# Performance work log

Measured on AMD Instinct MI355X. Metric: run time of the kernel, lower is better.

## Reference

```python
import jax, jax.numpy as jnp
import numpy as np

# ViT-Base-ish encoder: 256x256 img, patch 8 -> N=1024 tokens, dim 768, 8 layers
B, C, H, W = 8, 3, 256, 256
P, D, DEPTH, HEADS, DH, MLP = 8, 768, 8, 12, 64, 3072
N = (H // P) * (W // P)
INNER = HEADS * DH  # 768
EPS = 1e-5


def setup_inputs() -> dict:
    key = jax.random.key(0)
    ks = jax.random.split(key, 8)
    s = lambda i, shape, scale=0.02: jax.random.normal(ks[i], shape, jnp.float32) * scale
    return {
        "x": s(0, (B, C, H, W), 1.0),
        "w_conv": s(1, (D, C, P, P)),          # OIHW conv kernel (patch embed)
        "b_conv": jnp.zeros((D,), jnp.float32),
        "pos_emb": s(2, (1, N, D)),
        "ln1_w": jnp.ones((DEPTH, D), jnp.float32),
        "ln1_b": jnp.zeros((DEPTH, D), jnp.float32),
        "qkv_w": s(3, (DEPTH, D, 3 * INNER)),  # stored [in,out]; Linear has no bias
        "out_w": s(4, (DEPTH, INNER, D)),
        "out_b": jnp.zeros((DEPTH, D), jnp.float32),
        "ln2_w": jnp.ones((DEPTH, D), jnp.float32),
        "ln2_b": jnp.zeros((DEPTH, D), jnp.float32),
        "w1": s(5, (DEPTH, D, MLP)),
        "b1": jnp.zeros((DEPTH, MLP), jnp.float32),
        "w2": s(6, (DEPTH, MLP, D)),
        "b2": jnp.zeros((DEPTH, D), jnp.float32),
    }


def _layernorm(x, w, b):
    m = jnp.mean(x, axis=-1, keepdims=True)
    v = jnp.mean(jnp.square(x - m), axis=-1, keepdims=True)
    return (x - m) * jax.lax.rsqrt(v + EPS) * w + b


def _encoder(x, w_conv, b_conv, pos_emb, ln1_w, ln1_b, qkv_w, out_w, out_b,
             ln2_w, ln2_b, w1, b1, w2, b2):
    # PatchEmbed: strided conv -> flatten(2).transpose(1,2)
    h = jax.lax.conv_general_dilated(
        x, w_conv, window_strides=(P, P), padding='VALID',
        dimension_numbers=('NCHW', 'OIHW', 'NCHW'))
    h = h + b_conv[None, :, None, None]
    h = h.reshape(B, D, N).transpose(0, 2, 1)  # [B, N, D]
    h = h + pos_emb
    scale = DH ** -0.5

    def block(h, p):
        l1w, l1b, qkvw, ow, ob, l2w, l2b, W1, B1, W2, B2 = p
        # PreNorm + MHSA
        y = _layernorm(h, l1w, l1b)
        qkv = y @ qkvw                                   # [B,N,3*INNER]
        q, k, v = jnp.split(qkv, 3, axis=-1)
        split_heads = lambda t: t.reshape(B, N, HEADS, DH).transpose(0, 2, 1, 3)
        q, k, v = split_heads(q), split_heads(k), split_heads(v)
        attn = jax.nn.softmax(jnp.einsum('bhnd,bhmd->bhnm', q, k) * scale, axis=-1)
        o = jnp.einsum('bhnm,bhmd->bhnd', attn, v)
        o = o.transpose(0, 2, 1, 3).reshape(B, N, INNER)
        h = h + (o @ ow + ob)
        # PreNorm + FFN (exact GELU, dropout=0)
        y = _layernorm(h, l2w, l2b)
        h = h + (jax.nn.gelu(y @ W1 + B1, approximate=False) @ W2 + B2)
        return h, None

    h, _ = jax.lax.scan(block, h, (ln1_w, ln1_b, qkv_w, out_w, out_b,
                                   ln2_w, ln2_b, w1, b1, w2, b2))
    return h


def reference(x, w_conv, b_conv, pos_emb, ln1_w, ln1_b, qkv_w, out_w, out_b,
              ln2_w, ln2_b, w1, b1, w2, b2):
    return _encoder(x, w_conv, b_conv, pos_emb, ln1_w, ln1_b, qkv_w, out_w,
                    out_b, ln2_w, ln2_b, w1, b1, w2, b2)
```

## Files before the change

kernel.cpp:

```cpp
#include <hip/hip_runtime.h>
#include <math.h>

#define BATCH 8
#define CIN 3
#define HIMG 256
#define WIMG 256
#define PATCH 8
#define DMODEL 768
#define DEPTH 8
#define HEADS 12
#define DHEAD 64
#define MLPDIM 3072
#define NTOK 1024
#define INNER 768
#define MROWS (BATCH * NTOK)
#define QKVS (3 * INNER)
#define KPATCH (CIN * PATCH * PATCH)
#define LNEPS 1e-5f
#define PSTR 72
#define QSCALE 0.18033688011112042f

typedef __attribute__((ext_vector_type(8))) short short8;
typedef __attribute__((ext_vector_type(4))) float v4f;

__device__ __forceinline__ float b2f(unsigned short u) {
  union { unsigned int i; float f; } x;
  x.i = (unsigned int)u << 16;
  return x.f;
}
__device__ __forceinline__ unsigned short f2b(float f) {
  union { float f; unsigned int i; } x;
  x.f = f;
  unsigned int r = x.i + 0x7FFFu + ((x.i >> 16) & 1u);
  return (unsigned short)(r >> 16);
}
__device__ __forceinline__ unsigned int pkrh(float a, float b) {
  union { float f; unsigned int u; } x, y;
  x.f = a; y.f = b;
  return ((x.u + 0x8000u) >> 16) | ((y.u + 0x8000u) & 0xFFFF0000u);
}

#define GLL(gp, lp)                                                     \
  __builtin_amdgcn_global_load_lds(                                     \
      (const __attribute__((address_space(1))) void*)(gp),              \
      (__attribute__((address_space(3))) void*)(lp), 16, 0, 0)

__global__ __launch_bounds__(256) void cast_kernel(
    const float* __restrict__ src, unsigned short* __restrict__ dst, int n) {
  int i = blockIdx.x * 256 + threadIdx.x;
  if (i < n) dst[i] = f2b(src[i]);
}

__global__ __launch_bounds__(256) void transpose_cast_kernel(
    const float* __restrict__ src, unsigned short* __restrict__ dst, int R,
    int C) {
  __shared__ unsigned short t[32][33];
  src += (size_t)blockIdx.z * R * C;
  dst += (size_t)blockIdx.z * R * C;
  int c0 = blockIdx.x * 32, r0 = blockIdx.y * 32;
  int tx = threadIdx.x & 31, ty = threadIdx.x >> 5;
#pragma unroll
  for (int u = 0; u < 4; ++u) {
    int r = r0 + ty + u * 8;
    t[ty + u * 8][tx] = f2b(src[(size_t)r * C + c0 + tx]);
  }
  __syncthreads();
#pragma unroll
  for (int u = 0; u < 4; ++u) {
    int c = c0 + ty + u * 8;
    dst[(size_t)c * R + r0 + tx] = t[tx][ty + u * 8];
  }
}

__global__ __launch_bounds__(256) void vtrans_kernel(
    const unsigned short* __restrict__ qkv, unsigned short* __restrict__ vt) {
  __shared__ unsigned short t[32][33];
  int k0 = blockIdx.x * 32;
  int d0 = blockIdx.y * 32;
  int bh = blockIdx.z;
  int b = bh / HEADS, h = bh % HEADS;
  int tx = threadIdx.x & 31, ty = threadIdx.x >> 5;
  const unsigned short* src =
      qkv + (size_t)(b * NTOK) * QKVS + 2 * INNER + h * DHEAD;
#pragma unroll
  for (int u = 0; u < 4; ++u)
    t[ty + u * 8][tx] = src[(size_t)(k0 + ty + u * 8) * QKVS + d0 + tx];
  __syncthreads();
  unsigned short* dst = vt + ((size_t)bh * DHEAD + d0) * NTOK + k0;
#pragma unroll
  for (int u = 0; u < 4; ++u)
    dst[(size_t)(ty + u * 8) * NTOK + tx] = t[tx][ty + u * 8];
}

__global__ __launch_bounds__(256) void im2col_kernel(
    const float* __restrict__ x, unsigned short* __restrict__ A) {
  int idx = blockIdx.x * 256 + threadIdx.x;
  if (idx >= MROWS * KPATCH) return;
  int m = idx / KPATCH, k = idx % KPATCH;
  int b = m / NTOK, n = m % NTOK;
  int ph = n / 32, pw = n % 32;
  int c = k / 64, r = k % 64;
  int py = r / 8, px = r % 8;
  A[idx] =
      f2b(x[((size_t)(b * CIN + c) * HIMG + ph * 8 + py) * WIMG + pw * 8 + px]);
}

template <int EPI, int OB, int MT>
__global__ __launch_bounds__(256) void mfma_gemm_kernel(
    const unsigned short* __restrict__ Ag, const unsigned short* __restrict__ Bt,
    const float* __restrict__ bias, const float* __restrict__ res,
    void* __restrict__ Cg, int Mdim, int Ndim, int Kdim) {
  constexpr int MI = MT / 32;
  constexpr int RA = MT / 4;
  constexpr int NGA = RA / 16;
  __shared__ __align__(16) unsigned short Asm[MT * 32];
  __shared__ __align__(16) unsigned short Bsm[128 * 32];
  int tid = threadIdx.x;
  int lane = tid & 63, wv = tid >> 6;

  int Nt = Ndim / 128;
  int mchunk = (Mdim / MT) >> 3;
  int bid = blockIdx.x;
  int xcd = bid & 7;
  int j = bid >> 3;
  int m0 = (xcd * mchunk + j / Nt) * MT;
  int n0 = (j % Nt) * 128;

  v4f acc[MI][4] = {};
  int srow = lane >> 2, schunk = (lane & 3) * 8;

  const unsigned short* Aw = Ag + (size_t)(m0 + RA * wv + srow) * Kdim + schunk;
  const unsigned short* Bw = Bt + (size_t)(n0 + 32 * wv + srow) * Kdim + schunk;
  unsigned short* As0 = Asm + (RA * wv) * 32;
  unsigned short* Bs0 = Bsm + (32 * wv) * 32;

  int quad = lane >> 4, lr = lane & 15;
  int fr0 = (wv >> 1) * (MI * 16);
  int fc0 = (wv & 1) * 64;
  const unsigned short* Afr = Asm + (fr0 + lr) * 32 + quad * 8;
  const unsigned short* Bfr = Bsm + (fc0 + lr) * 32 + quad * 8;

  for (int k0 = 0; k0 < Kdim; k0 += 32) {
    GLL(Aw + k0, As0);
    if (NGA == 2) GLL(Aw + k0 + (size_t)16 * Kdim, As0 + 16 * 32);
    GLL(Bw + k0, Bs0);
    GLL(Bw + k0 + (size_t)16 * Kdim, Bs0 + 16 * 32);
    __syncthreads();
    short8 af[MI], bf[4];
#pragma unroll
    for (int i = 0; i < MI; ++i) af[i] = *(const short8*)(Afr + i * 16 * 32);
#pragma unroll
    for (int n = 0; n < 4; ++n) bf[n] = *(const short8*)(Bfr + n * 16 * 32);
#pragma unroll
    for (int i = 0; i < MI; ++i)
#pragma unroll
      for (int n = 0; n < 4; ++n)
        acc[i][n] = __builtin_amdgcn_mfma_f32_16x16x32_bf16(af[i], bf[n],
                                                            acc[i][n], 0, 0, 0);
    __syncthreads();
  }

  float* Cf = (float*)Cg;
  unsigned short* Cb = (unsigned short*)Cg;
#pragma unroll
  for (int i = 0; i < MI; ++i) {
#pragma unroll
    for (int n = 0; n < 4; ++n) {
      int ncol = n0 + fc0 + 16 * n + lr;
#pragma unroll
      for (int reg = 0; reg < 4; ++reg) {
        int mrow = m0 + fr0 + 16 * i + quad * 4 + reg;
        float v = acc[i][n][reg];
        if (EPI == 2 || EPI == 3 || EPI == 4) v += bias[ncol];
        if (EPI == 2) v += res[(size_t)mrow * Ndim + ncol];
        if (EPI == 3) {
          float u = v * (0.7978845608028654f + 0.035677408136300125f * v * v);
          float a = fminf(fmaxf(u * 2.8853900817779268f, -60.f), 60.f);
          float E = __builtin_amdgcn_exp2f(a);
          v = v * E * __builtin_amdgcn_rcpf(E + 1.0f);
        }
        if (EPI == 4) v += res[(size_t)(mrow % NTOK) * Ndim + ncol];
        if (EPI == 5 && ncol < INNER) v *= QSCALE;
        if (OB)
          Cb[(size_t)mrow * Ndim + ncol] = f2b(v);
        else
          Cf[(size_t)mrow * Ndim + ncol] = v;
      }
    }
  }
}

__global__ __launch_bounds__(256) void ln_kernel(
    const float* __restrict__ x, const float* __restrict__ w,
    const float* __restrict__ b, unsigned short* __restrict__ y) {
  int row = blockIdx.x;
  const float* xr = x + (size_t)row * DMODEL;
  unsigned short* yr = y + (size_t)row * DMODEL;
  int tid = threadIdx.x;
  float v0 = xr[tid], v1 = xr[tid + 256], v2 = xr[tid + 512];
  float s = v0 + v1 + v2;
  __shared__ float red[4];
#pragma unroll
  for (int off = 32; off >= 1; off >>= 1) s += __shfl_xor(s, off, 64);
  if ((tid & 63) == 0) red[tid >> 6] = s;
  __syncthreads();
  float mean = (red[0] + red[1] + red[2] + red[3]) * (1.0f / DMODEL);
  float d0 = v0 - mean, d1 = v1 - mean, d2 = v2 - mean;
  float sq = d0 * d0 + d1 * d1 + d2 * d2;
  __syncthreads();
#pragma unroll
  for (int off = 32; off >= 1; off >>= 1) sq += __shfl_xor(sq, off, 64);
  if ((tid & 63) == 0) red[tid >> 6] = sq;
  __syncthreads();
  float var = (red[0] + red[1] + red[2] + red[3]) * (1.0f / DMODEL);
  float rs = rsqrtf(var + LNEPS);
  yr[tid] = f2b(d0 * rs * w[tid] + b[tid]);
  yr[tid + 256] = f2b(d1 * rs * w[tid + 256] + b[tid + 256]);
  yr[tid + 512] = f2b(d2 * rs * w[tid + 512] + b[tid + 512]);
}

__global__ __launch_bounds__(256) void attn_kernel(
    const unsigned short* __restrict__ qkv,
    const unsigned short* __restrict__ vtg, unsigned short* __restrict__ o) {
  __shared__ __align__(16) unsigned short Ks[64 * PSTR];
  __shared__ __align__(16) unsigned short Vs[64 * PSTR];
  __shared__ __align__(16) unsigned short Pl[4][32 * PSTR];
  int tid = threadIdx.x;
  int lane = tid & 63, wv = tid >> 6;
  int quad = lane >> 4, lr = lane & 15;
  int q0 = blockIdx.x * 128, hh = blockIdx.y, bb = blockIdx.z;

  const unsigned short* qg =
      qkv + (size_t)(bb * NTOK + q0 + wv * 32) * QKVS + hh * DHEAD;
  const unsigned short* kg =
      qkv + (size_t)(bb * NTOK) * QKVS + INNER + hh * DHEAD;
  const unsigned short* vg = vtg + (size_t)(bb * HEADS + hh) * DHEAD * NTOK;
  unsigned short* Pw = Pl[wv];

  int srow = lane >> 3, soff = (lane & 7) * 8;

#pragma unroll
  for (int p = 0; p < 4; ++p) {
    int r = p * 8 + srow;
    *(int4*)(Pw + r * PSTR + soff) =
        *(const int4*)(qg + (size_t)r * QKVS + soff);
  }
  short8 qf[2][2];
#pragma unroll
  for (int n = 0; n < 2; ++n)
#pragma unroll
    for (int s = 0; s < 2; ++s)
      qf[n][s] =
          *(const short8*)(Pw + (n * 16 + lr) * PSTR + s * 32 + quad * 8);

  v4f oac[2][4] = {};
  float m_i[2] = {-1e30f, -1e30f};
  float l_i[2] = {0.f, 0.f};

  for (int t = 0; t < NTOK / 64; ++t) {
    __syncthreads();
#pragma unroll
    for (int p = 0; p < 2; ++p) {
      int r = wv * 16 + p * 8 + srow;
      *(int4*)(Ks + r * PSTR + soff) =
          *(const int4*)(kg + (size_t)(t * 64 + r) * QKVS + soff);
      *(int4*)(Vs + r * PSTR + soff) =
          *(const int4*)(vg + (size_t)r * NTOK + t * 64 + soff);
    }
    __syncthreads();

    v4f sac[4][2] = {};
#pragma unroll
    for (int s = 0; s < 2; ++s) {
      short8 kf[4];
#pragma unroll
      for (int mt = 0; mt < 4; ++mt)
        kf[mt] =
            *(const short8*)(Ks + (mt * 16 + lr) * PSTR + s * 32 + quad * 8);
#pragma unroll
      for (int mt = 0; mt < 4; ++mt)
#pragma unroll
        for (int n = 0; n < 2; ++n)
          sac[mt][n] = __builtin_amdgcn_mfma_f32_16x16x32_bf16(
              kf[mt], qf[n][s], sac[mt][n], 0, 0, 0);
    }

#pragma unroll
    for (int n = 0; n < 2; ++n) {
      float mx = -1e30f;
#pragma unroll
      for (int mt = 0; mt < 4; ++mt)
#pragma unroll
        for (int r = 0; r < 4; ++r) mx = fmaxf(mx, sac[mt][n][r]);
      mx = fmaxf(mx, __shfl_xor(mx, 16, 64));
      mx = fmaxf(mx, __shfl_xor(mx, 32, 64));
      float mnew = fmaxf(m_i[n], mx);
      float alpha = __builtin_amdgcn_exp2f(m_i[n] - mnew);
      m_i[n] = mnew;
      float sum = 0.f;
#pragma unroll
      for (int mt = 0; mt < 4; ++mt) {
#pragma unroll
        for (int r = 0; r < 4; ++r) {
          float p = __builtin_amdgcn_exp2f(sac[mt][n][r] - mnew);
          sac[mt][n][r] = p;
          sum += p;
        }
        *(uint2*)(Pw + (n * 16 + lr) * PSTR + mt * 16 + quad * 4) =
            make_uint2(pkrh(sac[mt][n][0], sac[mt][n][1]),
                       pkrh(sac[mt][n][2], sac[mt][n][3]));
      }
      sum += __shfl_xor(sum, 16, 64);
      sum += __shfl_xor(sum, 32, 64);
      l_i[n] = l_i[n] * alpha + sum;
#pragma unroll
      for (int r = 0; r < 4; ++r) {
        float ao = __shfl(alpha, quad * 4 + r, 64);
#pragma unroll
        for (int j = 0; j < 4; ++j) oac[n][j][r] *= ao;
      }
    }

#pragma unroll
    for (int s = 0; s < 2; ++s) {
      short8 pf[2], vf[4];
#pragma unroll
      for (int i = 0; i < 2; ++i)
        pf[i] =
            *(const short8*)(Pw + (i * 16 + lr) * PSTR + s * 32 + quad * 8);
#pragma unroll
      for (int j = 0; j < 4; ++j)
        vf[j] =
            *(const short8*)(Vs + (j * 16 + lr) * PSTR + s * 32 + quad * 8);
#pragma unroll
      for (int i = 0; i < 2; ++i)
#pragma unroll
        for (int j = 0; j < 4; ++j)
          oac[i][j] = __builtin_amdgcn_mfma_f32_16x16x32_bf16(
              pf[i], vf[j], oac[i][j], 0, 0, 0);
    }
  }

  unsigned short* ob =
      o + (size_t)(bb * NTOK + q0 + wv * 32) * INNER + hh * DHEAD;
#pragma unroll
  for (int i = 0; i < 2; ++i) {
    float inv = 1.0f / l_i[i];
#pragma unroll
    for (int r = 0; r < 4; ++r) {
      float il = __shfl(inv, quad * 4 + r, 64);
      int row = i * 16 + quad * 4 + r;
#pragma unroll
      for (int j = 0; j < 4; ++j)
        ob[(size_t)row * INNER + 16 * j + lr] = f2b(oac[i][j][r] * il);
    }
  }
}

extern "C" void kernel_launch(void* const* d_in, const int* in_sizes, int n_in,
                              void* d_out, int out_size, void* d_ws,
                              size_t ws_size, hipStream_t stream) {
  const float* x      = (const float*)d_in[0];
  const float* w_conv = (const float*)d_in[1];
  const float* b_conv = (const float*)d_in[2];
  const float* pos    = (const float*)d_in[3];
  const float* ln1w   = (const float*)d_in[4];
  const float* ln1b   = (const float*)d_in[5];
  const float* qkvw   = (const float*)d_in[6];
  const float* outw   = (const float*)d_in[7];
  const float* outb   = (const float*)d_in[8];
  const float* ln2w   = (const float*)d_in[9];
  const float* ln2b   = (const float*)d_in[10];
  const float* w1     = (const float*)d_in[11];
  const float* b1     = (const float*)d_in[12];
  const float* w2     = (const float*)d_in[13];
  const float* b2     = (const float*)d_in[14];

  char* ws = (char*)d_ws;
  float* outp = (float*)d_out;
  dim3 blk(256);

  float* h            = (float*)(ws + 0);
  unsigned short* big = (unsigned short*)(ws + 25165824);
  unsigned short* y   = (unsigned short*)(ws + 75497472);

  const size_t NEEDED = 214204416;
  bool batched = ws_size >= NEEDED;

  unsigned short *vt, *wc, *wqa, *woa, *w1a, *w2a;
  unsigned short *wq_f, *wo_f, *w1_f, *w2_f;
  if (batched) {
    vt  = (unsigned short*)(ws + 88080384);
    wc  = (unsigned short*)(ws + 100663296);
    wqa = (unsigned short*)(ws + 100958208);
    woa = (unsigned short*)(ws + 129269760);
    w1a = (unsigned short*)(ws + 138706944);
    w2a = (unsigned short*)(ws + 176455680);
    wq_f = wo_f = w1_f = w2_f = nullptr;
  } else {
    wq_f = (unsigned short*)(ws + 88080384);
    wo_f = (unsigned short*)(ws + 91619328);
    w1_f = (unsigned short*)(ws + 92798976);
    w2_f = (unsigned short*)(ws + 97517568);
    wc   = (unsigned short*)(ws + 102236160);
    vt   = (unsigned short*)(ws + 102531072);
    wqa = woa = w1a = w2a = nullptr;
  }

  cast_kernel<<<dim3((DMODEL * KPATCH + 255) / 256), blk, 0, stream>>>(
      w_conv, wc, DMODEL * KPATCH);
  im2col_kernel<<<dim3((MROWS * KPATCH + 255) / 256), blk, 0, stream>>>(x, big);
  mfma_gemm_kernel<4, 0, 64>
      <<<dim3((MROWS / 64) * (DMODEL / 128)), blk, 0, stream>>>(
          big, wc, b_conv, pos, h, MROWS, DMODEL, KPATCH);

  if (batched) {
    transpose_cast_kernel<<<dim3(QKVS / 32, DMODEL / 32, DEPTH), blk, 0,
                            stream>>>(qkvw, wqa, DMODEL, QKVS);
    transpose_cast_kernel<<<dim3(DMODEL / 32, INNER / 32, DEPTH), blk, 0,
                            stream>>>(outw, woa, INNER, DMODEL);
    transpose_cast_kernel<<<dim3(MLPDIM / 32, DMODEL / 32, DEPTH), blk, 0,
                            stream>>>(w1, w1a, DMODEL, MLPDIM);
    transpose_cast_kernel<<<dim3(DMODEL / 32, MLPDIM / 32, DEPTH), blk, 0,
                            stream>>>(w2, w2a, MLPDIM, DMODEL);
  }

  for (int l = 0; l < DEPTH; ++l) {
    unsigned short* wq = batched ? wqa + (size_t)l * DMODEL * QKVS : wq_f;
    unsigned short* wo = batched ? woa + (size_t)l * INNER * DMODEL : wo_f;
    unsigned short* w1t = batched ? w1a + (size_t)l * DMODEL * MLPDIM : w1_f;
    unsigned short* w2t = batched ? w2a + (size_t)l * MLPDIM * DMODEL : w2_f;
    if (!batched) {
      transpose_cast_kernel<<<dim3(QKVS / 32, DMODEL / 32), blk, 0, stream>>>(
          qkvw + (size_t)l * DMODEL * QKVS, wq, DMODEL, QKVS);
    }
    ln_kernel<<<dim3(MROWS), blk, 0, stream>>>(h, ln1w + l * DMODEL,
                                               ln1b + l * DMODEL, y);
    mfma_gemm_kernel<5, 1, 128>
        <<<dim3((MROWS / 128) * (QKVS / 128)), blk, 0, stream>>>(
            y, wq, nullptr, nullptr, big, MROWS, QKVS, DMODEL);
    vtrans_kernel<<<dim3(NTOK / 32, DHEAD / 32, BATCH * HEADS), blk, 0,
                    stream>>>(big, vt);
    attn_kernel<<<dim3(NTOK / 128, HEADS, BATCH), blk, 0, stream>>>(big, vt, y);
    if (!batched) {
      transpose_cast_kernel<<<dim3(DMODEL / 32, INNER / 32), blk, 0, stream>>>(
          outw + (size_t)l * INNER * DMODEL, wo, INNER, DMODEL);
    }
    mfma_gemm_kernel<2, 0, 64>
        <<<dim3((MROWS / 64) * (DMODEL / 128)), blk, 0, stream>>>(
            y, wo, outb + l * DMODEL, h, h, MROWS, DMODEL, INNER);
    ln_kernel<<<dim3(MROWS), blk, 0, stream>>>(h, ln2w + l * DMODEL,
                                               ln2b + l * DMODEL, y);
    if (!batched) {
      transpose_cast_kernel<<<dim3(MLPDIM / 32, DMODEL / 32), blk, 0, stream>>>(
          w1 + (size_t)l * DMODEL * MLPDIM, w1t, DMODEL, MLPDIM);
    }
    mfma_gemm_kernel<3, 1, 128>
        <<<dim3((MROWS / 128) * (MLPDIM / 128)), blk, 0, stream>>>(
            y, w1t, b1 + l * MLPDIM, nullptr, big, MROWS, MLPDIM, DMODEL);
    if (!batched) {
      transpose_cast_kernel<<<dim3(DMODEL / 32, MLPDIM / 32), blk, 0, stream>>>(
          w2 + (size_t)l * MLPDIM * DMODEL, w2t, MLPDIM, DMODEL);
    }
    float* dst = (l == DEPTH - 1) ? outp : h;
    mfma_gemm_kernel<2, 0, 64>
        <<<dim3((MROWS / 64) * (DMODEL / 128)), blk, 0, stream>>>(
            big, w2t, b2 + l * DMODEL, h, dst, MROWS, DMODEL, MLPDIM);
  }
}
```

Measured before the change: 2.543 ms.

## Double GEMM K-tile to 64 with XOR-swizzled LDS layout

The MFMA GEMM now stages a 64-wide K slice per iteration instead of 32, which halves the number of barrier pairs per K loop. The LDS tiles are stored with an XOR swizzle on the 16-byte chunk index, and the fragment reads use the same swizzle, to avoid bank conflicts from the wider row stride. The cost is doubled LDS use per block, which may reduce occupancy, and the kernel now needs Kdim to be a multiple of 64.

Result: faster. 2.215 ms (-12.9%).

```diff
diff --git a/kernel.cpp b/kernel.cpp
--- a/kernel.cpp
+++ b/kernel.cpp
@@ -112,9 +112,9 @@
     void* __restrict__ Cg, int Mdim, int Ndim, int Kdim) {
   constexpr int MI = MT / 32;
   constexpr int RA = MT / 4;
-  constexpr int NGA = RA / 16;
-  __shared__ __align__(16) unsigned short Asm[MT * 32];
-  __shared__ __align__(16) unsigned short Bsm[128 * 32];
+  constexpr int NCA = RA / 8;
+  __shared__ __align__(16) unsigned short Asm[MT * 64];
+  __shared__ __align__(16) unsigned short Bsm[128 * 64];
   int tid = threadIdx.x;
   int lane = tid & 63, wv = tid >> 6;
 
@@ -127,36 +127,46 @@
   int n0 = (j % Nt) * 128;
 
   v4f acc[MI][4] = {};
-  int srow = lane >> 2, schunk = (lane & 3) * 8;
-
-  const unsigned short* Aw = Ag + (size_t)(m0 + RA * wv + srow) * Kdim + schunk;
-  const unsigned short* Bw = Bt + (size_t)(n0 + 32 * wv + srow) * Kdim + schunk;
-  unsigned short* As0 = Asm + (RA * wv) * 32;
-  unsigned short* Bs0 = Bsm + (32 * wv) * 32;
+
+  int sr8 = lane >> 3;
+  int sc8 = ((lane & 7) ^ sr8) * 8;
+  const unsigned short* Aw = Ag + (size_t)(m0 + RA * wv + sr8) * Kdim + sc8;
+  const unsigned short* Bw = Bt + (size_t)(n0 + 32 * wv + sr8) * Kdim + sc8;
+  unsigned short* As0 = Asm + (RA * wv) * 64;
+  unsigned short* Bs0 = Bsm + (32 * wv) * 64;
 
   int quad = lane >> 4, lr = lane & 15;
   int fr0 = (wv >> 1) * (MI * 16);
   int fc0 = (wv & 1) * 64;
-  const unsigned short* Afr = Asm + (fr0 + lr) * 32 + quad * 8;
-  const unsigned short* Bfr = Bsm + (fc0 + lr) * 32 + quad * 8;
-
-  for (int k0 = 0; k0 < Kdim; k0 += 32) {
-    GLL(Aw + k0, As0);
-    if (NGA == 2) GLL(Aw + k0 + (size_t)16 * Kdim, As0 + 16 * 32);
-    GLL(Bw + k0, Bs0);
-    GLL(Bw + k0 + (size_t)16 * Kdim, Bs0 + 16 * 32);
+  int xcol = (quad ^ (lr & 7)) * 8;
+  const unsigned short* Afr = Asm + (fr0 + lr) * 64;
+  const unsigned short* Bfr = Bsm + (fc0 + lr) * 64;
+
+  for (int k0 = 0; k0 < Kdim; k0 += 64) {
+#pragma unroll
+    for (int c = 0; c < NCA; ++c)
+      GLL(Aw + k0 + (size_t)(8 * c) * Kdim, As0 + c * 8 * 64);
+#pragma unroll
+    for (int c = 0; c < 4; ++c)
+      GLL(Bw + k0 + (size_t)(8 * c) * Kdim, Bs0 + c * 8 * 64);
     __syncthreads();
-    short8 af[MI], bf[4];
-#pragma unroll
-    for (int i = 0; i < MI; ++i) af[i] = *(const short8*)(Afr + i * 16 * 32);
-#pragma unroll
-    for (int n = 0; n < 4; ++n) bf[n] = *(const short8*)(Bfr + n * 16 * 32);
-#pragma unroll
-    for (int i = 0; i < MI; ++i)
+#pragma unroll
+    for (int s = 0; s < 2; ++s) {
+      int xo = xcol ^ (s * 32);
+      short8 af[MI], bf[4];
+#pragma unroll
+      for (int i = 0; i < MI; ++i)
+        af[i] = *(const short8*)(Afr + i * 16 * 64 + xo);
 #pragma unroll
       for (int n = 0; n < 4; ++n)
-        acc[i][n] = __builtin_amdgcn_mfma_f32_16x16x32_bf16(af[i], bf[n],
-                                                            acc[i][n], 0, 0, 0);
+        bf[n] = *(const short8*)(Bfr + n * 16 * 64 + xo);
+#pragma unroll
+      for (int i = 0; i < MI; ++i)
+#pragma unroll
+        for (int n = 0; n < 4; ++n)
+          acc[i][n] = __builtin_amdgcn_mfma_f32_16x16x32_bf16(
+              af[i], bf[n], acc[i][n], 0, 0, 0);
+    }
     __syncthreads();
   }
 
```
